# Kernel optimization log

Measured on AMD Instinct MI355X. Metric: run time of the kernel, lower is better.

The kernel has to match this reference:

```python
import jax, jax.numpy as jnp
import numpy as np

B, T, D, H, HS = 4, 2048, 512, 8, 64

def setup_inputs() -> dict:
    key = jax.random.key(0)
    ks = jax.random.split(key, 5)
    scale = 1.0 / np.sqrt(D)
    return {
        "x": jax.random.normal(ks[0], (B, T, D), dtype=jnp.float32),
        "Wq": jax.random.normal(ks[1], (H, D, HS), dtype=jnp.float32) * scale,
        "Wk": jax.random.normal(ks[2], (H, D, HS), dtype=jnp.float32) * scale,
        "Wv": jax.random.normal(ks[3], (H, D, HS), dtype=jnp.float32) * scale,
        "Wo": jax.random.normal(ks[4], (D, D), dtype=jnp.float32) * scale,
        "bo": jnp.zeros((D,), dtype=jnp.float32),
    }

def reference(x, Wq, Wk, Wv, Wo, bo):
    # Per-head projections (stacked heads) -> [B,H,T,HS]
    q = jnp.einsum('btd,hde->bhte', x, Wq)
    k = jnp.einsum('btd,hde->bhte', x, Wk)
    v = jnp.einsum('btd,hde->bhte', x, Wv)
    # Full TxT attention scores, scaled by head_size**-0.5
    scores = jnp.einsum('bhte,bhse->bhts', q, k) * (HS ** -0.5)
    att = jax.nn.softmax(scores, axis=-1)
    out = jnp.einsum('bhts,bhse->bhte', att, v)
    # Concat heads: [B,H,T,HS] -> [B,T,H*HS] == [B,T,D]
    out = jnp.transpose(out, (0, 2, 1, 3)).reshape(out.shape[0], out.shape[2], -1)
    # Output projection (nn.Linear with bias)
    return out @ Wo + bo
```

## Files before the change

kernel.cpp:

```cpp
#include <hip/hip_runtime.h>
#include <stdint.h>

#define B_   4
#define T_   2048
#define D_   512
#define H_   8
#define HS_  64

typedef __attribute__((ext_vector_type(8))) short bf16x8;
typedef __attribute__((ext_vector_type(4))) float f32x4;

__device__ __forceinline__ unsigned short f2bf(float f) {
  union { float f; unsigned u; } v; v.f = f;
  unsigned r = v.u + 0x7fffu + ((v.u >> 16) & 1u);
  return (unsigned short)(r >> 16);
}

__device__ __forceinline__ void gload_lds16(const void* g, void* l) {
  __builtin_amdgcn_global_load_lds(
      (const __attribute__((address_space(1))) void*)g,
      (__attribute__((address_space(3))) void*)l,
      16, 0, 0);
}

__global__ __launch_bounds__(256) void k_prep(
    const float* __restrict__ x,
    const float* __restrict__ Wq, const float* __restrict__ Wk,
    const float* __restrict__ Wv, const float* __restrict__ Wo,
    unsigned short* __restrict__ xb, unsigned short* __restrict__ Wtq,
    unsigned short* __restrict__ Wto)
{
  const int bid = blockIdx.x, tid = threadIdx.x;
  if (bid < 4096) {
    const int i = bid * 256 + tid;
    float4 v = ((const float4*)x)[i];
    ushort4 o;
    o.x = f2bf(v.x); o.y = f2bf(v.y); o.z = f2bf(v.z); o.w = f2bf(v.w);
    ((ushort4*)xb)[i] = o;
  } else if (bid < 7168) {
    const int idx = (bid - 4096) * 256 + tid;
    const int n = idx >> 9, d = idx & 511;
    const int proj = n >> 9, c = n & 511, h = c >> 6, e = c & 63;
    const float* W = (proj == 0) ? Wq : ((proj == 1) ? Wk : Wv);
    Wtq[idx] = f2bf(W[((h << 9) + d) * 64 + e]);
  } else {
    const int idx = (bid - 7168) * 256 + tid;
    const int n = idx >> 9, d = idx & 511;
    Wto[idx] = f2bf(Wo[(d << 9) + n]);
  }
}

template<int MODE>
__global__ __launch_bounds__(256) void k_gemm(
    const unsigned short* __restrict__ A, const unsigned short* __restrict__ Bt,
    unsigned short* __restrict__ Qb, unsigned short* __restrict__ Kb,
    unsigned short* __restrict__ Vp,
    const float* __restrict__ bo, float* __restrict__ Cout)
{
  const int m0 = blockIdx.y * 128, n0 = blockIdx.x * 128;
  __shared__ unsigned short At[128 * 32];
  __shared__ unsigned short Bs[128 * 32];
  const int tid = threadIdx.x, lane = tid & 63, wid = tid >> 6;
  const int wm = wid >> 1, wn = wid & 1;
  const int r16 = lane & 15, g = lane >> 4;

  f32x4 acc[4][4];
  const f32x4 fz = {0.f, 0.f, 0.f, 0.f};
#pragma unroll
  for (int i = 0; i < 4; ++i)
#pragma unroll
    for (int j = 0; j < 4; ++j) acc[i][j] = fz;

  for (int k0 = 0; k0 < 512; k0 += 32) {
#pragma unroll
    for (int j = 0; j < 2; ++j) {
      const int idx = j * 256 + tid;
      const int rr = idx >> 2, cc = (idx & 3) << 3;
      gload_lds16(A + (size_t)(m0 + rr) * 512 + k0 + cc, &At[(j * 256 + wid * 64) * 8]);
      gload_lds16(Bt + (size_t)(n0 + rr) * 512 + k0 + cc, &Bs[(j * 256 + wid * 64) * 8]);
    }
    __syncthreads();
    bf16x8 am[4], bn[4];
#pragma unroll
    for (int mi = 0; mi < 4; ++mi)
      am[mi] = *(const bf16x8*)&At[(wm * 64 + mi * 16 + r16) * 32 + g * 8];
#pragma unroll
    for (int ni = 0; ni < 4; ++ni)
      bn[ni] = *(const bf16x8*)&Bs[(wn * 64 + ni * 16 + r16) * 32 + g * 8];
#pragma unroll
    for (int mi = 0; mi < 4; ++mi)
#pragma unroll
      for (int ni = 0; ni < 4; ++ni)
        acc[mi][ni] = __builtin_amdgcn_mfma_f32_16x16x32_bf16(am[mi], bn[ni], acc[mi][ni], 0, 0, 0);
    __syncthreads();
  }

  const float QSC = 0.18033688f;
#pragma unroll
  for (int mi = 0; mi < 4; ++mi) {
#pragma unroll
    for (int ni = 0; ni < 4; ++ni) {
      if (MODE == 0) {
        const int n = n0 + wn * 64 + ni * 16 + r16;
        const int proj = n >> 9, c = n & 511, h = c >> 6, e = c & 63;
        const int mbase = m0 + wm * 64 + mi * 16 + g * 4;
        const int b = mbase >> 11;
        if (proj == 2) {
          const int t0 = mbase & 2047;
          const int tblk = t0 >> 5;
          const int j0 = (g << 3) + ((mi & 1) << 2);
          ushort4 pv;
          pv.x = f2bf(acc[mi][ni][0]);
          pv.y = f2bf(acc[mi][ni][1]);
          pv.z = f2bf(acc[mi][ni][2]);
          pv.w = f2bf(acc[mi][ni][3]);
          *(ushort4*)&Vp[(((size_t)(b * 8 + h) << 6) + e) * 2048 + (tblk << 5) + j0] = pv;
        } else {
#pragma unroll
          for (int r = 0; r < 4; ++r) {
            const int m = mbase + r;
            const int t = m & 2047;
            const float val = acc[mi][ni][r];
            if (proj == 0)
              Qb[(((size_t)(b * 8 + h) * 2048 + t) << 6) + e] = f2bf(val * QSC);
            else
              Kb[(((size_t)(b * 8 + h) * 2048 + t) << 6) + e] = f2bf(val);
          }
        }
      } else {
#pragma unroll
        for (int r = 0; r < 4; ++r) {
          const int m = m0 + wm * 64 + mi * 16 + g * 4 + r;
          const int n = n0 + wn * 64 + ni * 16 + r16;
          Cout[(size_t)m * 512 + n] = acc[mi][ni][r] + bo[n];
        }
      }
    }
  }
}

#define DRAINBAR() do { \
    asm volatile("s_waitcnt vmcnt(0)" ::: "memory"); \
    __builtin_amdgcn_s_barrier(); \
    asm volatile("" ::: "memory"); } while (0)

__global__ __launch_bounds__(256, 3) void k_attn(
    const unsigned short* __restrict__ Qb, const unsigned short* __restrict__ Kb,
    const unsigned short* __restrict__ Vp, unsigned short* __restrict__ Ob)
{
  const int lin = blockIdx.x;
  const int xcd = lin & 7, slot = lin >> 3;
  const int bh = xcd * 4 + (slot & 3);
  const int qblk = slot >> 2;
  const int b = bh >> 3, h = bh & 7;

  const int tid = threadIdx.x, lane = tid & 63, wid = tid >> 6;
  const int q0 = qblk * 128 + wid * 32;
  const int r16 = lane & 15, g = lane >> 4;
  const int swz = r16 & 7;
  const unsigned short* Qh = Qb + (size_t)bh * T_ * 64;
  const unsigned short* Kh = Kb + (size_t)bh * T_ * 64;
  const unsigned short* Vh = Vp + (size_t)bh * 64 * T_;

  __shared__ unsigned short Ks[2][4096];
  __shared__ unsigned short Vs[2][4096];

  const bf16x8 qa00 = *(const bf16x8*)&Qh[(size_t)(q0 + r16) * 64 + g * 8];
  const bf16x8 qa01 = *(const bf16x8*)&Qh[(size_t)(q0 + r16) * 64 + 32 + g * 8];
  const bf16x8 qa10 = *(const bf16x8*)&Qh[(size_t)(q0 + 16 + r16) * 64 + g * 8];
  const bf16x8 qa11 = *(const bf16x8*)&Qh[(size_t)(q0 + 16 + r16) * 64 + 32 + g * 8];

  const f32x4 fz = {0.f, 0.f, 0.f, 0.f};
  f32x4 accA[4], accB[4];
#pragma unroll
  for (int eb = 0; eb < 4; ++eb) { accA[eb] = fz; accB[eb] = fz; }
  f32x4 accLA = fz, accLB = fz;

  bf16x8 onesv;
#pragma unroll
  for (int i = 0; i < 8; ++i) onesv[i] = (short)0x3F80;

  const int sb = wid * 8 + (lane >> 3);
  const int ssc = (lane & 7) ^ (lane >> 3);
  const unsigned short* kg = Kh + (size_t)sb * 64 + ssc * 8;
  const unsigned short* vg = Vh + (size_t)sb * T_ + ssc * 8;

  auto stage = [&](const unsigned short* kgp, const unsigned short* vgp, int bf) {
    gload_lds16(kgp,                   &Ks[bf][wid * 512]);
    gload_lds16(kgp + 32 * 64,         &Ks[bf][2048 + wid * 512]);
    gload_lds16(vgp,                   &Vs[bf][wid * 512]);
    gload_lds16(vgp + (size_t)32 * T_, &Vs[bf][2048 + wid * 512]);
  };

  auto compute = [&](int bf) {
#pragma unroll
    for (int sub = 0; sub < 2; ++sub) {
      const int rb = (sub * 32 + r16) * 64;
      const int c0 = (g ^ swz) << 3;
      const bf16x8 kf00 = *(const bf16x8*)&Ks[bf][rb + c0];
      const bf16x8 kf01 = *(const bf16x8*)&Ks[bf][rb + (c0 ^ 32)];
      const bf16x8 kf10 = *(const bf16x8*)&Ks[bf][rb + 1024 + c0];
      const bf16x8 kf11 = *(const bf16x8*)&Ks[bf][rb + 1024 + (c0 ^ 32)];
      f32x4 s0a = __builtin_amdgcn_mfma_f32_16x16x32_bf16(kf00, qa00, fz, 0, 0, 0);
      s0a = __builtin_amdgcn_mfma_f32_16x16x32_bf16(kf01, qa01, s0a, 0, 0, 0);
      f32x4 s1a = __builtin_amdgcn_mfma_f32_16x16x32_bf16(kf10, qa00, fz, 0, 0, 0);
      s1a = __builtin_amdgcn_mfma_f32_16x16x32_bf16(kf11, qa01, s1a, 0, 0, 0);
      f32x4 s0b = __builtin_amdgcn_mfma_f32_16x16x32_bf16(kf00, qa10, fz, 0, 0, 0);
      s0b = __builtin_amdgcn_mfma_f32_16x16x32_bf16(kf01, qa11, s0b, 0, 0, 0);
      f32x4 s1b = __builtin_amdgcn_mfma_f32_16x16x32_bf16(kf10, qa10, fz, 0, 0, 0);
      s1b = __builtin_amdgcn_mfma_f32_16x16x32_bf16(kf11, qa11, s1b, 0, 0, 0);

      float pa[8], pb[8];
#pragma unroll
      for (int r = 0; r < 4; ++r) {
        pa[r]     = __builtin_amdgcn_exp2f(s0a[r]);
        pa[4 + r] = __builtin_amdgcn_exp2f(s1a[r]);
        pb[r]     = __builtin_amdgcn_exp2f(s0b[r]);
        pb[4 + r] = __builtin_amdgcn_exp2f(s1b[r]);
      }
      union { bf16x8 v; unsigned u[4]; } puA, puB;
#pragma unroll
      for (int i = 0; i < 4; ++i) {
        asm("s_nop 1\n\tv_cvt_pk_bf16_f32 %0, %1, %2"
            : "=v"(puA.u[i]) : "v"(pa[2 * i]), "v"(pa[2 * i + 1]));
        asm("s_nop 1\n\tv_cvt_pk_bf16_f32 %0, %1, %2"
            : "=v"(puB.u[i]) : "v"(pb[2 * i]), "v"(pb[2 * i + 1]));
      }

#pragma unroll
      for (int eb = 0; eb < 4; ++eb) {
        const bf16x8 vf = *(const bf16x8*)&Vs[bf][(eb * 16 + r16) * 64 + (c0 ^ (sub << 5))];
        accA[eb] = __builtin_amdgcn_mfma_f32_16x16x32_bf16(vf, puA.v, accA[eb], 0, 0, 0);
        accB[eb] = __builtin_amdgcn_mfma_f32_16x16x32_bf16(vf, puB.v, accB[eb], 0, 0, 0);
      }
      accLA = __builtin_amdgcn_mfma_f32_16x16x32_bf16(onesv, puA.v, accLA, 0, 0, 0);
      accLB = __builtin_amdgcn_mfma_f32_16x16x32_bf16(onesv, puB.v, accLB, 0, 0, 0);
    }
  };

  stage(kg, vg, 0); kg += 4096; vg += 64;
  DRAINBAR();

#pragma unroll 1
  for (int t = 0; t < 32; t += 2) {
    stage(kg, vg, 1); kg += 4096; vg += 64;
    compute(0);
    DRAINBAR();
    if (t < 30) { stage(kg, vg, 0); kg += 4096; vg += 64; }
    compute(1);
    DRAINBAR();
  }

  const float invLA = 1.0f / accLA[0];
  const float invLB = 1.0f / accLB[0];
  unsigned short* OrowA = Ob + ((size_t)(b * 2048 + q0 + r16) << 9) + h * 64 + g * 4;
  unsigned short* OrowB = Ob + ((size_t)(b * 2048 + q0 + 16 + r16) << 9) + h * 64 + g * 4;
#pragma unroll
  for (int eb = 0; eb < 4; ++eb) {
    uint2 ow;
    asm("v_cvt_pk_bf16_f32 %0, %1, %2" : "=v"(ow.x)
        : "v"(accA[eb][0] * invLA), "v"(accA[eb][1] * invLA));
    asm("v_cvt_pk_bf16_f32 %0, %1, %2" : "=v"(ow.y)
        : "v"(accA[eb][2] * invLA), "v"(accA[eb][3] * invLA));
    *(uint2*)(OrowA + eb * 16) = ow;
    asm("v_cvt_pk_bf16_f32 %0, %1, %2" : "=v"(ow.x)
        : "v"(accB[eb][0] * invLB), "v"(accB[eb][1] * invLB));
    asm("v_cvt_pk_bf16_f32 %0, %1, %2" : "=v"(ow.y)
        : "v"(accB[eb][2] * invLB), "v"(accB[eb][3] * invLB));
    *(uint2*)(OrowB + eb * 16) = ow;
  }
}

extern "C" void kernel_launch(void* const* d_in, const int* in_sizes, int n_in,
                              void* d_out, int out_size, void* d_ws, size_t ws_size,
                              hipStream_t stream) {
  const float* x  = (const float*)d_in[0];
  const float* Wq = (const float*)d_in[1];
  const float* Wk = (const float*)d_in[2];
  const float* Wv = (const float*)d_in[3];
  const float* Wo = (const float*)d_in[4];
  const float* bo = (const float*)d_in[5];
  float* out = (float*)d_out;
  char* ws = (char*)d_ws;

  unsigned short* xb  = (unsigned short*)(ws);
  unsigned short* Wtq = (unsigned short*)(ws + 8388608);
  unsigned short* Wto = (unsigned short*)(ws + 9961472);
  unsigned short* Qb  = (unsigned short*)(ws + 10485760);
  unsigned short* Kb  = (unsigned short*)(ws + 18874368);
  unsigned short* Vp  = (unsigned short*)(ws + 27262976);
  unsigned short* Ob  = (unsigned short*)(ws + 35651584);

  k_prep    <<<8192, 256, 0, stream>>>(x, Wq, Wk, Wv, Wo, xb, Wtq, Wto);
  k_gemm<0> <<<dim3(12, 64), 256, 0, stream>>>(xb, Wtq, Qb, Kb, Vp, nullptr, nullptr);
  k_attn    <<<512, 256, 0, stream>>>(Qb, Kb, Vp, Ob);
  k_gemm<1> <<<dim3(4, 64), 256, 0, stream>>>(Ob, Wto, nullptr, nullptr, nullptr, bo, out);
}
```

Baseline: 95.07 us.

## Split attention KV range across two blocks and add combine kernel

The attention kernel now splits the key/value sequence in half, launching twice as many blocks. Each block writes unnormalized fp32 partial outputs and row sums to workspace. A new combine kernel adds the two halves, normalizes, and converts to bf16 for the output projection. This targets better occupancy and load balance on the MI355X's many CUs, at the cost of extra fp32 traffic (about 32MB written and read) plus one more kernel launch. The softmax uses no running max, so adding the two partials without rescaling is consistent with the existing code.

Result: slower. 101.0 us (+6.3%).

```diff
diff --git a/kernel.cpp b/kernel.cpp
--- a/kernel.cpp
+++ b/kernel.cpp
@@ -144,20 +144,23 @@
     __builtin_amdgcn_s_barrier(); \
     asm volatile("" ::: "memory"); } while (0)
 
-__global__ __launch_bounds__(256, 3) void k_attn(
+__global__ __launch_bounds__(256, 4) void k_attn(
     const unsigned short* __restrict__ Qb, const unsigned short* __restrict__ Kb,
-    const unsigned short* __restrict__ Vp, unsigned short* __restrict__ Ob)
+    const unsigned short* __restrict__ Vp, float* __restrict__ Opart,
+    float* __restrict__ Lp)
 {
   const int lin = blockIdx.x;
   const int xcd = lin & 7, slot = lin >> 3;
   const int bh = xcd * 4 + (slot & 3);
-  const int qblk = slot >> 2;
-  const int b = bh >> 3, h = bh & 7;
+  const int rest = slot >> 2;
+  const int z = rest & 1;
+  const int qblk = rest >> 1;
 
   const int tid = threadIdx.x, lane = tid & 63, wid = tid >> 6;
   const int q0 = qblk * 128 + wid * 32;
   const int r16 = lane & 15, g = lane >> 4;
   const int swz = r16 & 7;
+  const int kvb = z << 10;
   const unsigned short* Qh = Qb + (size_t)bh * T_ * 64;
   const unsigned short* Kh = Kb + (size_t)bh * T_ * 64;
   const unsigned short* Vh = Vp + (size_t)bh * 64 * T_;
@@ -182,8 +185,8 @@
 
   const int sb = wid * 8 + (lane >> 3);
   const int ssc = (lane & 7) ^ (lane >> 3);
-  const unsigned short* kg = Kh + (size_t)sb * 64 + ssc * 8;
-  const unsigned short* vg = Vh + (size_t)sb * T_ + ssc * 8;
+  const unsigned short* kg = Kh + (size_t)(kvb + sb) * 64 + ssc * 8;
+  const unsigned short* vg = Vh + (size_t)sb * T_ + kvb + ssc * 8;
 
   auto stage = [&](const unsigned short* kgp, const unsigned short* vgp, int bf) {
     gload_lds16(kgp,                   &Ks[bf][wid * 512]);
@@ -242,33 +245,46 @@
   DRAINBAR();
 
 #pragma unroll 1
-  for (int t = 0; t < 32; t += 2) {
+  for (int t = 0; t < 16; t += 2) {
     stage(kg, vg, 1); kg += 4096; vg += 64;
     compute(0);
     DRAINBAR();
-    if (t < 30) { stage(kg, vg, 0); kg += 4096; vg += 64; }
+    if (t < 14) { stage(kg, vg, 0); kg += 4096; vg += 64; }
     compute(1);
     DRAINBAR();
   }
 
-  const float invLA = 1.0f / accLA[0];
-  const float invLB = 1.0f / accLB[0];
-  unsigned short* OrowA = Ob + ((size_t)(b * 2048 + q0 + r16) << 9) + h * 64 + g * 4;
-  unsigned short* OrowB = Ob + ((size_t)(b * 2048 + q0 + 16 + r16) << 9) + h * 64 + g * 4;
+  const size_t rbA = ((size_t)(z * 32 + bh) * T_ + q0 + r16) * 64;
+  const size_t rbB = rbA + (size_t)16 * 64;
 #pragma unroll
   for (int eb = 0; eb < 4; ++eb) {
-    uint2 ow;
-    asm("v_cvt_pk_bf16_f32 %0, %1, %2" : "=v"(ow.x)
-        : "v"(accA[eb][0] * invLA), "v"(accA[eb][1] * invLA));
-    asm("v_cvt_pk_bf16_f32 %0, %1, %2" : "=v"(ow.y)
-        : "v"(accA[eb][2] * invLA), "v"(accA[eb][3] * invLA));
-    *(uint2*)(OrowA + eb * 16) = ow;
-    asm("v_cvt_pk_bf16_f32 %0, %1, %2" : "=v"(ow.x)
-        : "v"(accB[eb][0] * invLB), "v"(accB[eb][1] * invLB));
-    asm("v_cvt_pk_bf16_f32 %0, %1, %2" : "=v"(ow.y)
-        : "v"(accB[eb][2] * invLB), "v"(accB[eb][3] * invLB));
-    *(uint2*)(OrowB + eb * 16) = ow;
-  }
+    *(f32x4*)&Opart[rbA + eb * 16 + g * 4] = accA[eb];
+    *(f32x4*)&Opart[rbB + eb * 16 + g * 4] = accB[eb];
+  }
+  if (g == 0) {
+    Lp[(size_t)(z * 32 + bh) * T_ + q0 + r16]      = accLA[0];
+    Lp[(size_t)(z * 32 + bh) * T_ + q0 + 16 + r16] = accLB[0];
+  }
+}
+
+__global__ __launch_bounds__(256) void k_combine(
+    const float* __restrict__ Opart, const float* __restrict__ Lp,
+    unsigned short* __restrict__ Ob)
+{
+  const int i4 = blockIdx.x * 256 + threadIdx.x;
+  const size_t base = (size_t)i4 * 4;
+  const int e = (int)(base & 63), t = (int)((base >> 6) & 2047), bh = (int)(base >> 17);
+  const float L = Lp[(size_t)bh * T_ + t] + Lp[(size_t)(32 + bh) * T_ + t];
+  const float inv = 1.0f / L;
+  const f32x4 o0 = *(const f32x4*)&Opart[base];
+  const f32x4 o1 = *(const f32x4*)&Opart[4194304 + base];
+  ushort4 ow;
+  ow.x = f2bf((o0[0] + o1[0]) * inv);
+  ow.y = f2bf((o0[1] + o1[1]) * inv);
+  ow.z = f2bf((o0[2] + o1[2]) * inv);
+  ow.w = f2bf((o0[3] + o1[3]) * inv);
+  const int b = bh >> 3, h = bh & 7;
+  *(ushort4*)&Ob[((size_t)(b * 2048 + t) << 9) + h * 64 + e] = ow;
 }
 
 extern "C" void kernel_launch(void* const* d_in, const int* in_sizes, int n_in,
@@ -290,9 +306,12 @@
   unsigned short* Kb  = (unsigned short*)(ws + 18874368);
   unsigned short* Vp  = (unsigned short*)(ws + 27262976);
   unsigned short* Ob  = (unsigned short*)(ws + 35651584);
+  float*          Opart = (float*)(ws + 44040192);
+  float*          Lp    = (float*)(ws + 77594624);
 
   k_prep    <<<8192, 256, 0, stream>>>(x, Wq, Wk, Wv, Wo, xb, Wtq, Wto);
   k_gemm<0> <<<dim3(12, 64), 256, 0, stream>>>(xb, Wtq, Qb, Kb, Vp, nullptr, nullptr);
-  k_attn    <<<512, 256, 0, stream>>>(Qb, Kb, Vp, Ob);
+  k_attn    <<<1024, 256, 0, stream>>>(Qb, Kb, Vp, Opart, Lp);
+  k_combine <<<4096, 256, 0, stream>>>(Opart, Lp, Ob);
   k_gemm<1> <<<dim3(4, 64), 256, 0, stream>>>(Ob, Wto, nullptr, nullptr, nullptr, bo, out);
 }
```
